# Optimization experiments

Measured on AMD Instinct MI355X. Metric: run time of the kernel, lower is better.

Reference implementation:

```python
import jax, jax.numpy as jnp
import numpy as np

NUM_HEADS = 12
HEAD_DIM = 64
ROPE_THETA = 10000.0
WINDOW = 128  # local_attention: total window, +/- WINDOW//2 around each query
NEG_INF = jnp.finfo(jnp.float32).min


def _rotate_half(x):
    x1, x2 = jnp.split(x, 2, axis=-1)
    return jnp.concatenate([-x2, x1], axis=-1)


def _rope_cos_sin(position_ids, head_dim, theta):
    # position_ids: [B, S] int -> cos/sin: [B, S, head_dim]
    inv_freq = 1.0 / (theta ** (jnp.arange(0, head_dim, 2, dtype=jnp.float32) / head_dim))
    freqs = position_ids.astype(jnp.float32)[..., None] * inv_freq  # [B, S, hd/2]
    emb = jnp.concatenate([freqs, freqs], axis=-1)  # [B, S, hd]
    return jnp.cos(emb), jnp.sin(emb)


def setup_inputs() -> dict:
    key = jax.random.key(0)
    k1, k2, k3 = jax.random.split(key, 3)
    B, S, H = 4, 2048, 768
    hidden_states = jax.random.normal(k1, (B, S, H), dtype=jnp.float32)
    position_ids = jnp.broadcast_to(jnp.arange(S, dtype=jnp.int64), (B, S))
    Wqkv = jax.random.normal(k2, (3 * H, H), dtype=jnp.float32) * 0.02
    Wo = jax.random.normal(k3, (H, H), dtype=jnp.float32) * 0.02
    return {"hidden_states": hidden_states, "position_ids": position_ids, "Wqkv": Wqkv, "Wo": Wo}


def reference(hidden_states, position_ids, Wqkv, Wo):
    B, S, H = hidden_states.shape
    nh, hd = NUM_HEADS, HEAD_DIM
    # QKV projection (no bias, attention_bias=False)
    qkv = jnp.einsum("bsh,oh->bso", hidden_states, Wqkv)  # [B, S, 3H]
    qkv = qkv.reshape(B, S, 3, nh, hd)
    # torch: qkv.transpose(3,1).unbind(dim=2) -> q,k,v: [B, nh, S, hd]
    qkv = jnp.transpose(qkv, (0, 3, 2, 1, 4))
    query, key, value = qkv[:, :, 0], qkv[:, :, 1], qkv[:, :, 2]
    # RoPE (NeoX style, non-interleaved)
    cos, sin = _rope_cos_sin(position_ids, hd, ROPE_THETA)  # [B, S, hd]
    cos = cos[:, None]  # [B, 1, S, hd]
    sin = sin[:, None]
    query = query * cos + _rotate_half(query) * sin
    key = key * cos + _rotate_half(key) * sin
    # sliding-window additive mask: attend iff |i - j| <= WINDOW // 2
    idx = jnp.arange(S)
    in_window = jnp.abs(idx[:, None] - idx[None, :]) <= (WINDOW // 2)
    mask = jnp.where(in_window, 0.0, NEG_INF)[None, None]  # [1, 1, S, S]
    scale = hd ** (-0.5)
    scores = jnp.einsum("bhqd,bhkd->bhqk", query, key) * scale + mask
    attn = jax.nn.softmax(scores.astype(jnp.float32), axis=-1).astype(query.dtype)
    out = jnp.einsum("bhqk,bhkd->bhqd", attn, value)  # [B, nh, S, hd]
    out = jnp.transpose(out, (0, 2, 1, 3)).reshape(B, S, H)
    # output projection
    return jnp.einsum("bsh,oh->bso", out, Wo)
```

## Files before the change

### kernel.cpp

```cpp
#include <hip/hip_runtime.h>
#include <hip/hip_bf16.h>

#define Bn 4
#define Sn 2048
#define Hn 768
#define NHn 12
#define Mn (Bn*Sn)
#define QKVN 2304

typedef unsigned short u16;
typedef unsigned int u32;
typedef __attribute__((ext_vector_type(8))) short short8;
typedef __attribute__((ext_vector_type(4))) float f32x4;

typedef __attribute__((address_space(1))) const u32 g_u32;
typedef __attribute__((address_space(3))) u32 l_u32;

__device__ __forceinline__ void gll16(const void* g, void* l) {
    __builtin_amdgcn_global_load_lds((g_u32*)g, (l_u32*)l, 16, 0, 0);
}

__device__ __forceinline__ u16 f2bf(float f) {
    u32 x = __float_as_uint(f);
    x += 0x7fffu + ((x >> 16) & 1u);
    return (u16)(x >> 16);
}
__device__ __forceinline__ float bf2f(u16 u) {
    return __uint_as_float(((u32)u) << 16);
}

__global__ __launch_bounds__(256) void prep_k(const float* __restrict__ hs,
                                              const float* __restrict__ wqkv,
                                              const float* __restrict__ wo,
                                              const int* __restrict__ pos_ids,
                                              u16* __restrict__ hs_b,
                                              u16* __restrict__ wqkv_b,
                                              u16* __restrict__ wo_b,
                                              float2* __restrict__ tab) {
    int i = blockIdx.x * 256 + threadIdx.x;
    if (i < 262144) {
        int d2 = i & 31, row = i >> 5;
        float invf = exp2f((float)d2 * -0.4152410119f);
        float fr = (float)pos_ids[row] * invf;
        float sn, cs;
        sincosf(fr, &sn, &cs);
        tab[i] = make_float2(cs, sn);
        return;
    }
    i -= 262144;
    const float* s; u16* d; int off;
    if (i < 1572864)      { s = hs;   d = hs_b;   off = i; }
    else if (i < 2015232) { s = wqkv; d = wqkv_b; off = i - 1572864; }
    else if (i < 2162688) { s = wo;   d = wo_b;   off = i - 2015232; }
    else return;
    float4 v = ((const float4*)s)[off];
    ushort4 o;
    o.x = f2bf(v.x); o.y = f2bf(v.y); o.z = f2bf(v.z); o.w = f2bf(v.w);
    ((ushort4*)d)[off] = o;
}

#define KWAIT(N) do { \
    asm volatile("s_waitcnt vmcnt(" #N ")" ::: "memory"); \
    __builtin_amdgcn_s_barrier(); \
    __builtin_amdgcn_sched_barrier(0); \
} while (0)

__global__ __launch_bounds__(512, 2) void gemm_pipe(const u16* __restrict__ A,
                                                    const u16* __restrict__ Bw,
                                                    u16* __restrict__ C,
                                                    const float2* __restrict__ tab) {
    constexpr int K = 768, N = QKVN, NT = K / 32;
    __shared__ __align__(16) u16 As[4][256 * 32];
    __shared__ __align__(16) u16 Bs[4][256 * 32];
    const int t = threadIdx.x;
    const int wid = t >> 6, lane = t & 63;
    const int wm = wid >> 2, wn = wid & 3;
    const int lr = lane & 15, g = lane >> 4;

    int bid = blockIdx.x;
    int sw = (bid & 7) * 36 + (bid >> 3);
    const long m0 = (long)(sw / 9) * 256;
    const long n0 = (long)(sw % 9) * 256;

    f32x4 acc[8][4] = {};

    auto stageA = [&](int slot, int kt) {
        #pragma unroll
        for (int j = 0; j < 2; ++j) {
            int idx = t + j * 512;
            int row = idx >> 2, gg = idx & 3;
            int col8 = (gg ^ ((row >> 1) & 3)) * 8;
            gll16(A + (m0 + row) * K + kt * 32 + col8, (char*)As[slot] + idx * 16);
        }
    };
    auto stageB = [&](int slot, int kt) {
        #pragma unroll
        for (int j = 0; j < 2; ++j) {
            int idx = t + j * 512;
            int row = idx >> 2, gg = idx & 3;
            int col8 = (gg ^ ((row >> 1) & 3)) * 8;
            gll16(Bw + (n0 + row) * K + kt * 32 + col8, (char*)Bs[slot] + idx * 16);
        }
    };

    auto computeTile = [&](int slot, int kstage) {
        const u16* Ab = As[slot];
        const u16* Bb = Bs[slot];
        short8 bf_[4], af_[4];
        #pragma unroll
        for (int nf = 0; nf < 4; ++nf) {
            int row = wn * 64 + nf * 16 + lr;
            bf_[nf] = *(const short8*)((const char*)Bb + row * 64 +
                                       ((g ^ ((row >> 1) & 3)) << 4));
        }
        #pragma unroll
        for (int mf = 0; mf < 4; ++mf) {
            int row = wm * 128 + mf * 16 + lr;
            af_[mf] = *(const short8*)((const char*)Ab + row * 64 +
                                       ((g ^ ((row >> 1) & 3)) << 4));
        }
        if (kstage >= 0) stageA(kstage & 3, kstage);
        __builtin_amdgcn_s_barrier();
        __builtin_amdgcn_s_setprio(1);
        #pragma unroll
        for (int mf = 0; mf < 4; ++mf)
            #pragma unroll
            for (int nf = 0; nf < 4; ++nf)
                acc[mf][nf] = __builtin_amdgcn_mfma_f32_16x16x32_bf16(
                    af_[mf], bf_[nf], acc[mf][nf], 0, 0, 0);
        __builtin_amdgcn_s_setprio(0);
        __builtin_amdgcn_s_barrier();
        #pragma unroll
        for (int mf = 0; mf < 4; ++mf) {
            int row = wm * 128 + 64 + mf * 16 + lr;
            af_[mf] = *(const short8*)((const char*)Ab + row * 64 +
                                       ((g ^ ((row >> 1) & 3)) << 4));
        }
        if (kstage >= 0) stageB(kstage & 3, kstage);
        __builtin_amdgcn_s_barrier();
        __builtin_amdgcn_s_setprio(1);
        #pragma unroll
        for (int mf = 0; mf < 4; ++mf)
            #pragma unroll
            for (int nf = 0; nf < 4; ++nf)
                acc[mf + 4][nf] = __builtin_amdgcn_mfma_f32_16x16x32_bf16(
                    af_[mf], bf_[nf], acc[mf + 4][nf], 0, 0, 0);
        __builtin_amdgcn_s_setprio(0);
    };

    stageA(0, 0); stageB(0, 0);
    stageA(1, 1); stageB(1, 1);
    stageA(2, 2); stageB(2, 2);

    for (int it = 0; it <= NT - 4; ++it) {
        KWAIT(8);
        computeTile(it & 3, it + 3);
    }
    KWAIT(8); computeTile((NT - 3) & 3, -1);
    KWAIT(4); computeTile((NT - 2) & 3, -1);
    KWAIT(0); computeTile((NT - 1) & 3, -1);

    if ((n0 + wn * 64) < 1536) {
        #pragma unroll
        for (int mf = 0; mf < 8; ++mf)
            #pragma unroll
            for (int r = 0; r < 4; ++r) {
                long row = m0 + wm * 128 + mf * 16 + g * 4 + r;
                const float2* tr = tab + row * 32;
                #pragma unroll
                for (int ntp = 0; ntp < 2; ++ntp) {
                    float2 cssn = tr[ntp * 16 + lr];
                    float x1 = acc[mf][ntp][r], x2 = acc[mf][ntp + 2][r];
                    acc[mf][ntp][r]     = x1 * cssn.x - x2 * cssn.y;
                    acc[mf][ntp + 2][r] = x2 * cssn.x + x1 * cssn.y;
                }
            }
    }

    #pragma unroll
    for (int mf = 0; mf < 8; ++mf)
        #pragma unroll
        for (int nf = 0; nf < 4; ++nf)
            #pragma unroll
            for (int r = 0; r < 4; ++r) {
                long row = m0 + wm * 128 + mf * 16 + g * 4 + r;
                long col = n0 + wn * 64 + nf * 16 + lr;
                C[row * N + col] = f2bf(acc[mf][nf][r]);
            }
}

template <int BM, int BN, typename OUT>
__global__ __launch_bounds__(256, 4) void gemm_bt(const u16* __restrict__ A,
                                                  const u16* __restrict__ Bw,
                                                  OUT* __restrict__ C,
                                                  int N, int K) {
    constexpr int WM = BM / 2, WN = BN / 2;
    constexpr int MR = WM / 16, NR = WN / 16;
    __shared__ __align__(16) u16 As[BM * 64];
    __shared__ __align__(16) u16 Bs[BN * 64];
    const int t = threadIdx.x;
    const int wid = t >> 6, lane = t & 63;
    const int wr = wid >> 1, wc = wid & 1;
    const long m0 = (long)blockIdx.x * BM;
    const long n0 = (long)blockIdx.y * BN;
    const int lr = lane & 15, g = lane >> 4;

    f32x4 acc[MR][NR] = {};

    for (int kt = 0; kt < K; kt += 64) {
        #pragma unroll
        for (int ss = 0; ss < BM / 32; ++ss) {
            int s = t + ss * 256;
            int row = s >> 3, gg = s & 7;
            int col8 = (gg ^ (row & 7)) * 8;
            gll16(A + (m0 + row) * K + kt + col8, (char*)As + s * 16);
        }
        #pragma unroll
        for (int ss = 0; ss < BN / 32; ++ss) {
            int s = t + ss * 256;
            int row = s >> 3, gg = s & 7;
            int col8 = (gg ^ (row & 7)) * 8;
            gll16(Bw + (n0 + row) * K + kt + col8, (char*)Bs + s * 16);
        }
        __syncthreads();
        #pragma unroll
        for (int kk2 = 0; kk2 < 2; ++kk2) {
            const int slot = kk2 * 4 + g;
            short8 bfr[NR];
            #pragma unroll
            for (int nt = 0; nt < NR; ++nt) {
                int row = wc * WN + nt * 16 + lr;
                bfr[nt] = *(const short8*)((const char*)Bs + row * 128 +
                                           ((slot ^ (row & 7)) << 4));
            }
            #pragma unroll
            for (int mt = 0; mt < MR; ++mt) {
                int row = wr * WM + mt * 16 + lr;
                short8 af = *(const short8*)((const char*)As + row * 128 +
                                             ((slot ^ (row & 7)) << 4));
                #pragma unroll
                for (int nt = 0; nt < NR; ++nt)
                    acc[mt][nt] = __builtin_amdgcn_mfma_f32_16x16x32_bf16(
                        af, bfr[nt], acc[mt][nt], 0, 0, 0);
            }
        }
        __syncthreads();
    }

    #pragma unroll
    for (int mt = 0; mt < MR; ++mt)
        #pragma unroll
        for (int nt = 0; nt < NR; ++nt)
            #pragma unroll
            for (int r = 0; r < 4; ++r) {
                long row = m0 + wr * WM + mt * 16 + g * 4 + r;
                long col = n0 + wc * WN + nt * 16 + lr;
                float v = acc[mt][nt][r];
                if constexpr (sizeof(OUT) == 2) C[row * N + col] = (OUT)f2bf(v);
                else                            C[row * N + col] = v;
            }
}

__global__ __launch_bounds__(256) void attn_k(const u16* __restrict__ qkv,
                                              u16* __restrict__ outb) {
    const int qt = blockIdx.x, bh = blockIdx.y;
    const int b = bh / NHn, h = bh % NHn;
    const int q0 = qt * 64, kv0 = q0 - 64;
    const int t = threadIdx.x, wid = t >> 6, lane = t & 63;
    const int lr = lane & 15, g = lane >> 4;

    __shared__ __align__(16) char smem[58368];
    u16* Qs = (u16*)smem;
    u16* Ks = (u16*)(smem + 8192);
    u16* Vt = (u16*)(smem + 32768);

    const size_t rowbase = (size_t)b * Sn;

    #pragma unroll
    for (int ss = 0; ss < 2; ++ss) {
        int s = t + ss * 256;
        int row = s >> 3, gg = s & 7;
        int col8 = (gg ^ (row & 7)) * 8;
        gll16(qkv + (rowbase + q0 + row) * QKVN + h * 64 + col8, (char*)Qs + s * 16);
    }
    #pragma unroll
    for (int ss = 0; ss < 6; ++ss) {
        int s = t + ss * 256;
        int row = s >> 3, gg = s & 7;
        int kk = kv0 + row;
        kk = kk < 0 ? 0 : (kk > Sn - 1 ? Sn - 1 : kk);
        int col8 = (gg ^ (row & 7)) * 8;
        gll16(qkv + (rowbase + kk) * QKVN + 768 + h * 64 + col8, (char*)Ks + s * 16);
    }
    #pragma unroll
    for (int ss = 0; ss < 6; ++ss) {
        int s = t + ss * 256;
        int krow = s >> 3, gg = s & 7;
        int kk = kv0 + krow;
        kk = kk < 0 ? 0 : (kk > Sn - 1 ? Sn - 1 : kk);
        short8 v = *(const short8*)(qkv + (rowbase + kk) * QKVN + 1536 + h * 64 + gg * 8);
        #pragma unroll
        for (int j = 0; j < 8; ++j) Vt[(gg * 8 + j) * 200 + krow] = (u16)v[j];
    }
    __syncthreads();

    f32x4 sacc[12] = {};
    #pragma unroll
    for (int kk2 = 0; kk2 < 2; ++kk2) {
        int qrow = wid * 16 + lr;
        int slot = kk2 * 4 + g;
        short8 qf = *(const short8*)((const char*)Qs + qrow * 128 + ((slot ^ (qrow & 7)) << 4));
        #pragma unroll
        for (int tl = 0; tl < 12; ++tl) {
            int krow = tl * 16 + lr;
            short8 kf = *(const short8*)((const char*)Ks + krow * 128 + ((slot ^ (krow & 7)) << 4));
            sacc[tl] = __builtin_amdgcn_mfma_f32_16x16x32_bf16(qf, kf, sacc[tl], 0, 0, 0);
        }
    }

    float p[12][4];
    float lsum[4];
    #pragma unroll
    for (int r = 0; r < 4; ++r) {
        int qq = q0 + wid * 16 + g * 4 + r;
        float mx = -3.0e38f;
        #pragma unroll
        for (int tl = 0; tl < 12; ++tl) {
            int kq = kv0 + tl * 16 + lr;
            float sc = sacc[tl][r] * 0.125f;
            int dqk = qq - kq;
            bool valid = (kq >= 0) && (kq < Sn) && (dqk <= 64) && (dqk >= -64);
            sc = valid ? sc : -3.0e38f;
            p[tl][r] = sc;
            mx = fmaxf(mx, sc);
        }
        #pragma unroll
        for (int mk = 1; mk < 16; mk <<= 1) mx = fmaxf(mx, __shfl_xor(mx, mk, 16));
        float sum = 0.f;
        #pragma unroll
        for (int tl = 0; tl < 12; ++tl) {
            float e = __expf(p[tl][r] - mx);
            p[tl][r] = e;
            sum += e;
        }
        #pragma unroll
        for (int mk = 1; mk < 16; mk <<= 1) sum += __shfl_xor(sum, mk, 16);
        lsum[r] = sum;
    }

    __syncthreads();

    u16* Pw = (u16*)(smem + wid * 6400);
    #pragma unroll
    for (int tl = 0; tl < 12; ++tl)
        #pragma unroll
        for (int r = 0; r < 4; ++r)
            Pw[(g * 4 + r) * 200 + tl * 16 + lr] = f2bf(p[tl][r]);

    f32x4 oacc[4] = {};
    #pragma unroll
    for (int ks = 0; ks < 6; ++ks) {
        short8 pf = *(const short8*)((const char*)Pw + lr * 400 + (ks * 32 + g * 8) * 2);
        #pragma unroll
        for (int dt = 0; dt < 4; ++dt) {
            short8 vf = *(const short8*)((const char*)Vt + (dt * 16 + lr) * 400 + (ks * 32 + g * 8) * 2);
            oacc[dt] = __builtin_amdgcn_mfma_f32_16x16x32_bf16(pf, vf, oacc[dt], 0, 0, 0);
        }
    }

    #pragma unroll
    for (int dt = 0; dt < 4; ++dt)
        #pragma unroll
        for (int r = 0; r < 4; ++r) {
            int row = q0 + wid * 16 + g * 4 + r;
            float v = oacc[dt][r] / lsum[r];
            outb[(rowbase + row) * Hn + h * 64 + dt * 16 + lr] = f2bf(v);
        }
}

extern "C" void kernel_launch(void* const* d_in, const int* in_sizes, int n_in,
                              void* d_out, int out_size, void* d_ws, size_t ws_size,
                              hipStream_t stream) {
    const float* hs   = (const float*)d_in[0];
    const int*   pos  = (const int*)d_in[1];
    const float* wqkv = (const float*)d_in[2];
    const float* wo   = (const float*)d_in[3];
    float* out = (float*)d_out;
    char* ws = (char*)d_ws;

    u16* hs_b   = (u16*)(ws);
    u16* wqkv_b = (u16*)(ws + 12582912);
    u16* wo_b   = (u16*)(ws + 16121856);
    u16* qkv    = (u16*)(ws + 17301504);
    u16* attn   = (u16*)(ws + 55050240);
    float2* tab = (float2*)(ws + 55050240);

    prep_k<<<9472, 256, 0, stream>>>(hs, wqkv, wo, pos, hs_b, wqkv_b, wo_b, tab);

    gemm_pipe<<<288, 512, 0, stream>>>(hs_b, wqkv_b, qkv, tab);

    attn_k<<<dim3(32, 48), 256, 0, stream>>>(qkv, attn);

    gemm_bt<128, 64, float><<<dim3(64, 12), 256, 0, stream>>>(
        attn, wo_b, out, 768, 768);
}
```

Measured before the change: 122.7 us.

## Simplify QKV GEMM pipeline to 3-stage buffer with single compute phase

The QKV projection GEMM drops from a 4-slot to a 3-slot LDS ring with a prefetch distance of two tiles. Each k-tile now loads all eight A fragments and issues all MFMAs in one phase instead of two halves separated by barriers. The XCD-aware block swizzle is replaced by a plain m-major block mapping. This cuts LDS use and intra-tile barriers, at the cost of less prefetch depth, more live registers, and possibly worse L2 locality from the unswizzled mapping.

```diff
diff --git a/kernel.cpp b/kernel.cpp
--- a/kernel.cpp
+++ b/kernel.cpp
@@ -28,6 +28,12 @@
 __device__ __forceinline__ float bf2f(u16 u) {
     return __uint_as_float(((u32)u) << 16);
 }
+
+#define KWAIT(N) do { \
+    asm volatile("s_waitcnt vmcnt(" #N ")" ::: "memory"); \
+    __builtin_amdgcn_s_barrier(); \
+    __builtin_amdgcn_sched_barrier(0); \
+} while (0)
 
 __global__ __launch_bounds__(256) void prep_k(const float* __restrict__ hs,
                                               const float* __restrict__ wqkv,
@@ -59,32 +65,24 @@
     ((ushort4*)d)[off] = o;
 }
 
-#define KWAIT(N) do { \
-    asm volatile("s_waitcnt vmcnt(" #N ")" ::: "memory"); \
-    __builtin_amdgcn_s_barrier(); \
-    __builtin_amdgcn_sched_barrier(0); \
-} while (0)
-
-__global__ __launch_bounds__(512, 2) void gemm_pipe(const u16* __restrict__ A,
-                                                    const u16* __restrict__ Bw,
-                                                    u16* __restrict__ C,
-                                                    const float2* __restrict__ tab) {
+__global__ __launch_bounds__(512, 2) void gemm256(const u16* __restrict__ A,
+                                                  const u16* __restrict__ Bw,
+                                                  u16* __restrict__ C,
+                                                  const float2* __restrict__ tab) {
     constexpr int K = 768, N = QKVN, NT = K / 32;
-    __shared__ __align__(16) u16 As[4][256 * 32];
-    __shared__ __align__(16) u16 Bs[4][256 * 32];
+    __shared__ __align__(16) u16 As[3][256 * 32];
+    __shared__ __align__(16) u16 Bs[3][256 * 32];
     const int t = threadIdx.x;
     const int wid = t >> 6, lane = t & 63;
     const int wm = wid >> 2, wn = wid & 3;
     const int lr = lane & 15, g = lane >> 4;
 
-    int bid = blockIdx.x;
-    int sw = (bid & 7) * 36 + (bid >> 3);
-    const long m0 = (long)(sw / 9) * 256;
-    const long n0 = (long)(sw % 9) * 256;
+    const long m0 = (long)(blockIdx.x & 31) * 256;
+    const long n0 = (long)(blockIdx.x >> 5) * 256;
 
     f32x4 acc[8][4] = {};
 
-    auto stageA = [&](int slot, int kt) {
+    auto stage = [&](int slot, int kt) {
         #pragma unroll
         for (int j = 0; j < 2; ++j) {
             int idx = t + j * 512;
@@ -92,8 +90,6 @@
             int col8 = (gg ^ ((row >> 1) & 3)) * 8;
             gll16(A + (m0 + row) * K + kt * 32 + col8, (char*)As[slot] + idx * 16);
         }
-    };
-    auto stageB = [&](int slot, int kt) {
         #pragma unroll
         for (int j = 0; j < 2; ++j) {
             int idx = t + j * 512;
@@ -103,62 +99,45 @@
         }
     };
 
-    auto computeTile = [&](int slot, int kstage) {
+    auto compute = [&](int slot, int stslot, int kstage) {
         const u16* Ab = As[slot];
         const u16* Bb = Bs[slot];
-        short8 bf_[4], af_[4];
+        short8 af[8], bfr[4];
         #pragma unroll
         for (int nf = 0; nf < 4; ++nf) {
             int row = wn * 64 + nf * 16 + lr;
-            bf_[nf] = *(const short8*)((const char*)Bb + row * 64 +
+            bfr[nf] = *(const short8*)((const char*)Bb + row * 64 +
                                        ((g ^ ((row >> 1) & 3)) << 4));
         }
         #pragma unroll
-        for (int mf = 0; mf < 4; ++mf) {
+        for (int mf = 0; mf < 8; ++mf) {
             int row = wm * 128 + mf * 16 + lr;
-            af_[mf] = *(const short8*)((const char*)Ab + row * 64 +
-                                       ((g ^ ((row >> 1) & 3)) << 4));
-        }
-        if (kstage >= 0) stageA(kstage & 3, kstage);
-        __builtin_amdgcn_s_barrier();
+            af[mf] = *(const short8*)((const char*)Ab + row * 64 +
+                                      ((g ^ ((row >> 1) & 3)) << 4));
+        }
+        if (kstage >= 0) stage(stslot, kstage);
         __builtin_amdgcn_s_setprio(1);
         #pragma unroll
-        for (int mf = 0; mf < 4; ++mf)
+        for (int mf = 0; mf < 8; ++mf)
             #pragma unroll
             for (int nf = 0; nf < 4; ++nf)
                 acc[mf][nf] = __builtin_amdgcn_mfma_f32_16x16x32_bf16(
-                    af_[mf], bf_[nf], acc[mf][nf], 0, 0, 0);
-        __builtin_amdgcn_s_setprio(0);
-        __builtin_amdgcn_s_barrier();
-        #pragma unroll
-        for (int mf = 0; mf < 4; ++mf) {
-            int row = wm * 128 + 64 + mf * 16 + lr;
-            af_[mf] = *(const short8*)((const char*)Ab + row * 64 +
-                                       ((g ^ ((row >> 1) & 3)) << 4));
-        }
-        if (kstage >= 0) stageB(kstage & 3, kstage);
-        __builtin_amdgcn_s_barrier();
-        __builtin_amdgcn_s_setprio(1);
-        #pragma unroll
-        for (int mf = 0; mf < 4; ++mf)
-            #pragma unroll
-            for (int nf = 0; nf < 4; ++nf)
-                acc[mf + 4][nf] = __builtin_amdgcn_mfma_f32_16x16x32_bf16(
-                    af_[mf], bf_[nf], acc[mf + 4][nf], 0, 0, 0);
+                    af[mf], bfr[nf], acc[mf][nf], 0, 0, 0);
         __builtin_amdgcn_s_setprio(0);
     };
 
-    stageA(0, 0); stageB(0, 0);
-    stageA(1, 1); stageB(1, 1);
-    stageA(2, 2); stageB(2, 2);
-
-    for (int it = 0; it <= NT - 4; ++it) {
-        KWAIT(8);
-        computeTile(it & 3, it + 3);
-    }
-    KWAIT(8); computeTile((NT - 3) & 3, -1);
-    KWAIT(4); computeTile((NT - 2) & 3, -1);
-    KWAIT(0); computeTile((NT - 1) & 3, -1);
+    stage(0, 0);
+    stage(1, 1);
+    int sl = 0;
+    for (int it = 0; it + 2 < NT; ++it) {
+        KWAIT(4);
+        int s2 = sl + 2; if (s2 >= 3) s2 -= 3;
+        compute(sl, s2, it + 2);
+        ++sl; if (sl == 3) sl = 0;
+    }
+    KWAIT(4); compute(sl, 0, -1);
+    ++sl; if (sl == 3) sl = 0;
+    KWAIT(0); compute(sl, 0, -1);
 
     if ((n0 + wn * 64) < 1536) {
         #pragma unroll
@@ -397,7 +376,7 @@
 
     prep_k<<<9472, 256, 0, stream>>>(hs, wqkv, wo, pos, hs_b, wqkv_b, wo_b, tab);
 
-    gemm_pipe<<<288, 512, 0, stream>>>(hs_b, wqkv_b, qkv, tab);
+    gemm256<<<288, 512, 0, stream>>>(hs_b, wqkv_b, qkv, tab);
 
     attn_k<<<dim3(32, 48), 256, 0, stream>>>(qkv, attn);
 
```

New measurement: 104.6 us. 14.7% less time.
